# Optimization experiments

Hardware: AMD Instinct MI355X
Metric: run time of the kernel (lower is better)

The kernel has to match this reference:

```python
import jax, jax.numpy as jnp
import numpy as np

B, N, F = 4, 256, 128
H = 256  # hidden width of readout MLP
OUT = 1


def setup_inputs() -> dict:
    key = jax.random.key(0)
    k_x, k_wp, k_w1, k_b1, k_w2, k_b2 = jax.random.split(key, 6)
    node_embeddings = jax.random.normal(k_x, (B, N, F), dtype=jnp.float32)
    # layer_pooled: Linear(F, F, bias=False); stored as [in, out]
    W_pool = jax.random.normal(k_wp, (F, F), dtype=jnp.float32) / np.sqrt(F)
    # readout layer 1: Linear(3F, H, bias=True)
    W1 = jax.random.normal(k_w1, (3 * F, H), dtype=jnp.float32) / np.sqrt(3 * F)
    b1 = jax.random.normal(k_b1, (H,), dtype=jnp.float32) * 0.01
    # readout layer 2: Linear(H, OUT, bias=True)
    W2 = jax.random.normal(k_w2, (H, OUT), dtype=jnp.float32) / np.sqrt(H)
    b2 = jax.random.normal(k_b2, (OUT,), dtype=jnp.float32) * 0.01
    return {"node_embeddings": node_embeddings, "W_pool": W_pool,
            "W1": W1, "b1": b1, "W2": W2, "b2": b2}


def reference(node_embeddings, W_pool, W1, b1, W2, b2):
    b, n, f = node_embeddings.shape
    # pooled context: mean over nodes, then Linear(F,F) (no bias)
    h_pooled = jnp.einsum('bf,fh->bh', node_embeddings.mean(axis=1), W_pool)  # [B,F]
    # pairwise grid: features[b,i,j] = relu(concat(h_pooled[b], x[b,i], x[b,j]))
    f_pooled = jnp.broadcast_to(h_pooled[:, None, None, :], (b, n, n, f))
    f_i = jnp.broadcast_to(node_embeddings[:, :, None, :], (b, n, n, f))  # f_expanded
    f_j = jnp.broadcast_to(node_embeddings[:, None, :, :], (b, n, n, f))  # f_expanded_diff
    features = jax.nn.relu(jnp.concatenate([f_pooled, f_i, f_j], axis=-1))  # [B,N,N,3F]
    h = jax.nn.relu(jnp.einsum('bijk,kh->bijh', features, W1) + b1)  # [B,N,N,H]
    out = jnp.einsum('bijh,ho->bijo', h, W2) + b2  # [B,N,N,OUT]
    return out
```

## Files before the change

### kernel.cpp

```cpp
#include <hip/hip_runtime.h>
#include <hip/hip_bf16.h>

#define B 4
#define N 256
#define F 128
#define H 256

__global__ __launch_bounds__(256) void kAW(
    const float* __restrict__ x, const float* __restrict__ Wp,
    const float* __restrict__ W1, const float* __restrict__ b1,
    float* __restrict__ ub, float* __restrict__ A, float* __restrict__ W) {
  __shared__ float xr[2][F];
  const int blk = blockIdx.x;
  const int b = blk >> 7;
  const int i0 = (blk & 127) * 2;
  const int t = threadIdx.x;

  {
    const int r = t >> 7, f = t & 127;
    xr[r][f] = fmaxf(x[(b * N + i0 + r) * F + f], 0.f);
  }
  __syncthreads();

  float a0 = 0.f, a1 = 0.f, w0 = 0.f, w1 = 0.f;
  const float* W1i = W1 + F * H;
  const float* W1j = W1 + 2 * F * H;
#pragma unroll 8
  for (int f = 0; f < F; ++f) {
    const float wi = W1i[f * H + t];
    const float wj = W1j[f * H + t];
    const float x0 = xr[0][f];
    const float x1 = xr[1][f];
    a0 = fmaf(x0, wi, a0);
    a1 = fmaf(x1, wi, a1);
    w0 = fmaf(x0, wj, w0);
    w1 = fmaf(x1, wj, w1);
  }
  A[(b * N + i0) * H + t] = a0;
  A[(b * N + i0 + 1) * H + t] = a1;
  W[(b * N + i0) * H + t] = w0;
  W[(b * N + i0 + 1) * H + t] = w1;

  if (blk < B) {
    __shared__ float4 red4[256];
    __shared__ float xm_s[F];
    __shared__ float rp_s[F];
    __shared__ float part[256];
    const int pb = blk;
    const float4* xb4 = (const float4*)(x + pb * N * F);
    float4 acc = make_float4(0.f, 0.f, 0.f, 0.f);
#pragma unroll 8
    for (int k = 0; k < 32; ++k) {
      const float4 v = xb4[t + 256 * k];
      acc.x += v.x; acc.y += v.y; acc.z += v.z; acc.w += v.w;
    }
    red4[t] = acc;
    __syncthreads();
    if (t < 32) {
      float4 s = red4[t];
#pragma unroll
      for (int m = 1; m < 8; ++m) {
        const float4 v = red4[t + 32 * m];
        s.x += v.x; s.y += v.y; s.z += v.z; s.w += v.w;
      }
      const float inv = 1.f / (float)N;
      xm_s[4 * t + 0] = s.x * inv;
      xm_s[4 * t + 1] = s.y * inv;
      xm_s[4 * t + 2] = s.z * inv;
      xm_s[4 * t + 3] = s.w * inv;
    }
    __syncthreads();
    {
      const int lo = t & 127, kh = t >> 7;
      float p = 0.f;
      const int k0 = kh * 64;
#pragma unroll 8
      for (int kk = 0; kk < 64; ++kk) {
        const int k = k0 + kk;
        p = fmaf(xm_s[k], Wp[k * F + lo], p);
      }
      part[t] = p;
    }
    __syncthreads();
    if (t < 128) rp_s[t] = fmaxf(part[t] + part[t + 128], 0.f);
    __syncthreads();
    {
      float u = b1[t];
#pragma unroll 8
      for (int k = 0; k < F; ++k) u = fmaf(rp_s[k], W1[k * H + t], u);
      ub[pb * H + t] = u;
    }
  }
}

#define SA 34
#define SW 17
__global__ __launch_bounds__(256) void kPair(
    const float* __restrict__ A, const float* __restrict__ W,
    const float* __restrict__ ub, const float* __restrict__ W2,
    const float* __restrict__ b2, float* __restrict__ out) {
  __shared__ float aT[256 * SA];
  __shared__ float wT[256 * SW];
  __shared__ float w2s[256];

  const int b = blockIdx.z;
  const int i0 = blockIdx.y * 32;
  const int j0 = blockIdx.x * 16;
  const int t = threadIdx.x;

  w2s[t] = W2[t];
  const float ubv = ub[b * H + t];

  const float* Ab = A + (b * N + i0) * H;
#pragma unroll 8
  for (int r = 0; r < 32; ++r)
    aT[t * SA + r] = Ab[r * H + t] + ubv;

  const float* Wb = W + (b * N + j0) * H;
#pragma unroll 8
  for (int r = 0; r < 16; ++r)
    wT[t * SW + r] = Wb[r * H + t];
  __syncthreads();

  const int ti = t >> 3;
  const int tj = t & 7;
  float acc0 = 0.f, acc1 = 0.f;
#pragma unroll 8
  for (int h = 0; h < 256; ++h) {
    const float a  = aT[h * SA + ti];
    const float v0 = wT[h * SW + 2 * tj];
    const float v1 = wT[h * SW + 2 * tj + 1];
    const float w2 = w2s[h];
    acc0 = fmaf(fmaxf(a + v0, 0.f), w2, acc0);
    acc1 = fmaf(fmaxf(a + v1, 0.f), w2, acc1);
  }

  const float bb = b2[0];
  float* o = out + (b * N + i0 + ti) * N + j0 + 2 * tj;
  o[0] = acc0 + bb;
  o[1] = acc1 + bb;
}

extern "C" void kernel_launch(void* const* d_in, const int* in_sizes, int n_in,
                              void* d_out, int out_size, void* d_ws, size_t ws_size,
                              hipStream_t stream) {
  const float* x  = (const float*)d_in[0];
  const float* Wp = (const float*)d_in[1];
  const float* W1 = (const float*)d_in[2];
  const float* b1 = (const float*)d_in[3];
  const float* W2 = (const float*)d_in[4];
  const float* b2 = (const float*)d_in[5];
  float* out = (float*)d_out;

  float* ws = (float*)d_ws;
  float* ub = ws;
  float* A  = ub + B * H;
  float* W  = A + B * N * H;

  kAW<<<dim3(B * N / 2), dim3(256), 0, stream>>>(x, Wp, W1, b1, ub, A, W);
  kPair<<<dim3(N / 16, N / 32, B), dim3(256), 0, stream>>>(A, W, ub, W2, b2, out);
}
```

Measured before the change: 89.13 us.

## Fuse projection and pairwise kernels into one cooperative launch with grid sync

Merges the per-node projection kernel and the pairwise readout kernel into a single cooperative kernel of 256 blocks, separated by a grid-wide barrier. Each block now projects 4 nodes instead of 2, and in the pairwise phase each thread computes a 2x2 output tile using float2 shared loads on 32x32 tiles. The aim is to remove a kernel launch and raise arithmetic intensity per shared-memory load. In exchange it needs a cooperative launch and a grid sync, and it cuts the pairwise grid to 256 blocks, which may limit parallelism.

Measured after the change: 134.1 us. +50.5%, slower.

```diff
diff --git a/kernel.cpp b/kernel.cpp
--- a/kernel.cpp
+++ b/kernel.cpp
@@ -1,51 +1,70 @@
 #include <hip/hip_runtime.h>
 #include <hip/hip_bf16.h>
+#include <hip/hip_cooperative_groups.h>
+
+namespace cg = cooperative_groups;
 
 #define B 4
 #define N 256
 #define F 128
 #define H 256
 
-__global__ __launch_bounds__(256) void kAW(
+#define SA 34
+
+__global__ __launch_bounds__(256) void kFused(
     const float* __restrict__ x, const float* __restrict__ Wp,
     const float* __restrict__ W1, const float* __restrict__ b1,
-    float* __restrict__ ub, float* __restrict__ A, float* __restrict__ W) {
-  __shared__ float xr[2][F];
+    const float* __restrict__ W2, const float* __restrict__ b2,
+    float* __restrict__ ub, float* __restrict__ A, float* __restrict__ W,
+    float* __restrict__ out) {
+  __shared__ float xr[4][F];
+  __shared__ float aT[256 * SA];
+  __shared__ float wT[256 * SA];
+  __shared__ float w2s[H];
+  __shared__ float4 red4[256];
+  __shared__ float xm_s[F];
+  __shared__ float rp_s[F];
+  __shared__ float part[256];
+
   const int blk = blockIdx.x;
-  const int b = blk >> 7;
-  const int i0 = (blk & 127) * 2;
   const int t = threadIdx.x;
+  const int b = blk >> 6;
 
+  const int i0 = (blk & 63) * 4;
   {
     const int r = t >> 7, f = t & 127;
-    xr[r][f] = fmaxf(x[(b * N + i0 + r) * F + f], 0.f);
+    xr[r][f]     = fmaxf(x[(b * N + i0 + r) * F + f], 0.f);
+    xr[r + 2][f] = fmaxf(x[(b * N + i0 + r + 2) * F + f], 0.f);
   }
   __syncthreads();
 
-  float a0 = 0.f, a1 = 0.f, w0 = 0.f, w1 = 0.f;
-  const float* W1i = W1 + F * H;
-  const float* W1j = W1 + 2 * F * H;
-#pragma unroll 8
-  for (int f = 0; f < F; ++f) {
-    const float wi = W1i[f * H + t];
-    const float wj = W1j[f * H + t];
-    const float x0 = xr[0][f];
-    const float x1 = xr[1][f];
-    a0 = fmaf(x0, wi, a0);
-    a1 = fmaf(x1, wi, a1);
-    w0 = fmaf(x0, wj, w0);
-    w1 = fmaf(x1, wj, w1);
+  {
+    float a0 = 0.f, a1 = 0.f, a2 = 0.f, a3 = 0.f;
+    float q0 = 0.f, q1 = 0.f, q2 = 0.f, q3 = 0.f;
+    const float* W1i = W1 + F * H;
+    const float* W1j = W1 + 2 * F * H;
+#pragma unroll 4
+    for (int f = 0; f < F; ++f) {
+      const float wi = W1i[f * H + t];
+      const float wj = W1j[f * H + t];
+      const float x0 = xr[0][f], x1 = xr[1][f];
+      const float x2 = xr[2][f], x3 = xr[3][f];
+      a0 = fmaf(x0, wi, a0); a1 = fmaf(x1, wi, a1);
+      a2 = fmaf(x2, wi, a2); a3 = fmaf(x3, wi, a3);
+      q0 = fmaf(x0, wj, q0); q1 = fmaf(x1, wj, q1);
+      q2 = fmaf(x2, wj, q2); q3 = fmaf(x3, wj, q3);
+    }
+    A[(b * N + i0 + 0) * H + t] = a0;
+    A[(b * N + i0 + 1) * H + t] = a1;
+    A[(b * N + i0 + 2) * H + t] = a2;
+    A[(b * N + i0 + 3) * H + t] = a3;
+    W[(b * N + i0 + 0) * H + t] = q0;
+    W[(b * N + i0 + 1) * H + t] = q1;
+    W[(b * N + i0 + 2) * H + t] = q2;
+    W[(b * N + i0 + 3) * H + t] = q3;
   }
-  A[(b * N + i0) * H + t] = a0;
-  A[(b * N + i0 + 1) * H + t] = a1;
-  W[(b * N + i0) * H + t] = w0;
-  W[(b * N + i0 + 1) * H + t] = w1;
 
   if (blk < B) {
-    __shared__ float4 red4[256];
-    __shared__ float xm_s[F];
-    __shared__ float rp_s[F];
-    __shared__ float part[256];
     const int pb = blk;
     const float4* xb4 = (const float4*)(x + pb * N * F);
     float4 acc = make_float4(0.f, 0.f, 0.f, 0.f);
@@ -91,54 +110,49 @@
       ub[pb * H + t] = u;
     }
   }
-}
 
-#define SA 34
-#define SW 17
-__global__ __launch_bounds__(256) void kPair(
-    const float* __restrict__ A, const float* __restrict__ W,
-    const float* __restrict__ ub, const float* __restrict__ W2,
-    const float* __restrict__ b2, float* __restrict__ out) {
-  __shared__ float aT[256 * SA];
-  __shared__ float wT[256 * SW];
-  __shared__ float w2s[256];
+  cg::this_grid().sync();
 
-  const int b = blockIdx.z;
-  const int i0 = blockIdx.y * 32;
-  const int j0 = blockIdx.x * 16;
-  const int t = threadIdx.x;
+  const int jt = blk & 7;
+  const int it = (blk >> 3) & 7;
+  const int i0b = it * 32;
+  const int j0b = jt * 32;
 
   w2s[t] = W2[t];
   const float ubv = ub[b * H + t];
-
-  const float* Ab = A + (b * N + i0) * H;
+  const float* Ab = A + (b * N + i0b) * H;
+  const float* Wb = W + (b * N + j0b) * H;
 #pragma unroll 8
-  for (int r = 0; r < 32; ++r)
+  for (int r = 0; r < 32; ++r) {
     aT[t * SA + r] = Ab[r * H + t] + ubv;
-
-  const float* Wb = W + (b * N + j0) * H;
-#pragma unroll 8
-  for (int r = 0; r < 16; ++r)
-    wT[t * SW + r] = Wb[r * H + t];
+    wT[t * SA + r] = Wb[r * H + t];
+  }
   __syncthreads();
 
-  const int ti = t >> 3;
-  const int tj = t & 7;
-  float acc0 = 0.f, acc1 = 0.f;
+  const int tj = t & 15;
+  const int ti = t >> 4;
+  float acc00 = 0.f, acc01 = 0.f, acc10 = 0.f, acc11 = 0.f;
+  const float* ap = aT + 2 * ti;
+  const float* wp = wT + 2 * tj;
 #pragma unroll 8
   for (int h = 0; h < 256; ++h) {
-    const float a  = aT[h * SA + ti];
-    const float v0 = wT[h * SW + 2 * tj];
-    const float v1 = wT[h * SW + 2 * tj + 1];
-    const float w2 = w2s[h];
-    acc0 = fmaf(fmaxf(a + v0, 0.f), w2, acc0);
-    acc1 = fmaf(fmaxf(a + v1, 0.f), w2, acc1);
+    const float2 av = *(const float2*)(ap + h * SA);
+    const float2 wv = *(const float2*)(wp + h * SA);
+    const float w2h = w2s[h];
+    acc00 = fmaf(fmaxf(av.x + wv.x, 0.f), w2h, acc00);
+    acc01 = fmaf(fmaxf(av.x + wv.y, 0.f), w2h, acc01);
+    acc10 = fmaf(fmaxf(av.y + wv.x, 0.f), w2h, acc10);
+    acc11 = fmaf(fmaxf(av.y + wv.y, 0.f), w2h, acc11);
   }
 
   const float bb = b2[0];
-  float* o = out + (b * N + i0 + ti) * N + j0 + 2 * tj;
-  o[0] = acc0 + bb;
-  o[1] = acc1 + bb;
+  const int i = i0b + 2 * ti;
+  const int j = j0b + 2 * tj;
+  float* o0 = out + (b * N + i) * N + j;
+  o0[0] = acc00 + bb;
+  o0[1] = acc01 + bb;
+  o0[N] = acc10 + bb;
+  o0[N + 1] = acc11 + bb;
 }
 
 extern "C" void kernel_launch(void* const* d_in, const int* in_sizes, int n_in,
@@ -157,6 +171,9 @@
   float* A  = ub + B * H;
   float* W  = A + B * N * H;
 
-  kAW<<<dim3(B * N / 2), dim3(256), 0, stream>>>(x, Wp, W1, b1, ub, A, W);
-  kPair<<<dim3(N / 16, N / 32, B), dim3(256), 0, stream>>>(A, W, ub, W2, b2, out);
+  void* args[] = {(void*)&x, (void*)&Wp, (void*)&W1, (void*)&b1,
+                  (void*)&W2, (void*)&b2, (void*)&ub, (void*)&A,
+                  (void*)&W, (void*)&out};
+  hipLaunchCooperativeKernel((const void*)kFused, dim3(256), dim3(256),
+                             args, 0, stream);
 }
```
